# Performance work log

Measured on AMD Instinct MI355X. Metric: run time of the kernel, lower is better.

Reference implementation:

```python
import jax, jax.numpy as jnp
import numpy as np

P = 10      # qubits
LQ = 4      # re-uploading layers
B = 4096    # batch
HID = 32    # readout hidden
DIM = 2 ** P


def _rz(t):
    t = jnp.asarray(t, jnp.float32)
    e = jnp.exp(-0.5j * t.astype(jnp.complex64))
    z = jnp.zeros_like(e)
    return jnp.stack([jnp.stack([e, z], -1), jnp.stack([z, jnp.conj(e)], -1)], -2)


def _rx(t):
    t = jnp.asarray(t, jnp.float32)
    c = jnp.cos(0.5 * t).astype(jnp.complex64)
    s = jnp.sin(0.5 * t).astype(jnp.complex64)
    return jnp.stack([jnp.stack([c, -1j * s], -1), jnp.stack([-1j * s, c], -1)], -2)


def _ry(t):
    t = jnp.asarray(t, jnp.float32)
    c = jnp.cos(0.5 * t).astype(jnp.complex64)
    s = jnp.sin(0.5 * t).astype(jnp.complex64)
    return jnp.stack([jnp.stack([c, -s], -1), jnp.stack([s, c], -1)], -2)


def _apply_1q(state, U, k):
    # state [B, 2^P] complex, U [B,2,2]; wire 0 = most-significant bit (PennyLane order)
    b = state.shape[0]
    s = state.reshape(b, 2 ** k, 2, -1)
    s = jnp.einsum('bij,bajc->baic', U, s)
    return s.reshape(b, -1)


def _apply_cnot(state, c, t):
    b = state.shape[0]
    a, d = min(c, t), max(c, t)
    s = state.reshape(b, 2 ** a, 2, 2 ** (d - a - 1), 2, -1)
    if c == a:  # control = smaller wire index (axis 2), target at axis 4
        hi = jnp.flip(s[:, :, 1], axis=3)  # [b,pre,mid,2,post] -> flip target bit
        s = jnp.stack([s[:, :, 0], hi], axis=2)
    else:       # control = larger wire index (axis 4), target at axis 2
        hi = jnp.flip(s[:, :, :, :, 1], axis=2)  # [b,pre,2,mid,post] -> flip target bit
        s = jnp.stack([s[:, :, :, :, 0], hi], axis=4)
    return s.reshape(b, -1)


def _meas_signs(p):
    # rows 0..p-1: Z_k signs; rows p..2p-1: Z_k Z_{(k+1)%p} signs
    idx = np.arange(2 ** p)
    bits = (idx[None, :] >> (p - 1 - np.arange(p)[:, None])) & 1
    z = (1.0 - 2.0 * bits).astype(np.float32)            # [p, 2^p]
    zz = z * np.roll(z, -1, axis=0)                      # [p, 2^p]
    return jnp.asarray(np.concatenate([z, zz], axis=0))  # [2p, 2^p]


MEAS = _meas_signs(P)


def _circuit_feats(theta, rot_weights, enc_scale, enc_bias):
    b = theta.shape[0]
    # Hadamard on every wire of |0...0> -> uniform superposition
    state = jnp.full((b, DIM), 1.0 / np.sqrt(DIM), dtype=jnp.complex64)
    for l in range(LQ):
        for k in range(P):
            t0 = enc_scale[l, k, 0] * theta[:, k] + enc_bias[l, k, 0]
            t1 = enc_scale[l, k, 1] * theta[:, k] + enc_bias[l, k, 1]
            U_enc = jnp.einsum('bij,bjk->bik', _rx(t1), _rz(t0))  # RX(t1) RZ(t0)
            w = rot_weights[l, k]
            # PennyLane Rot(phi,theta,omega) = RZ(omega) RY(theta) RZ(phi)
            U_rot = _rz(w[2]) @ _ry(w[1]) @ _rz(w[0])
            U = jnp.einsum('ij,bjk->bik', U_rot, U_enc)
            state = _apply_1q(state, U, k)
        for k in range(P):
            state = _apply_cnot(state, k, (k + 1) % P)
    probs = jnp.abs(state) ** 2              # [B, 2^P]
    return probs @ MEAS.T                    # [B, 2P] expectation values


def setup_inputs() -> dict:
    key = jax.random.key(0)
    ks = jax.random.split(key, 4)
    theta = jax.random.uniform(ks[0], (B, P), jnp.float32, -np.pi, np.pi)
    rot_weights = 0.02 * jax.random.normal(ks[1], (LQ, P, 3), dtype=jnp.float32)
    enc_scale = jnp.ones((LQ, P, 2), jnp.float32)   # clamp(0.5,1.5) of ones = ones
    enc_bias = jnp.zeros((LQ, P, 2), jnp.float32)
    n_meas = 2 * P
    W1 = jax.random.normal(ks[2], (HID, n_meas), dtype=jnp.float32) / np.sqrt(n_meas)
    b1 = jnp.zeros((HID,), jnp.float32)
    W2 = jax.random.normal(ks[3], (1, HID), dtype=jnp.float32) / np.sqrt(HID)
    b2 = jnp.zeros((1,), jnp.float32)
    return dict(theta=theta, rot_weights=rot_weights, enc_scale=enc_scale,
                enc_bias=enc_bias, W1=W1, b1=b1, W2=W2, b2=b2)


def reference(theta, rot_weights, enc_scale, enc_bias, W1, b1, W2, b2):
    feats = _circuit_feats(theta, rot_weights, enc_scale, enc_bias)
    h = jax.nn.silu(feats @ W1.T + b1)
    return (h @ W2.T + b2)[:, 0]  # [B]
```

## Files before the change

kernel.cpp:

```cpp
#include <hip/hip_runtime.h>
#include <math.h>

#define NQ   10
#define NLAY 4
#define BATCH 4096
#define HID  32
#define NM   20

typedef float f2 __attribute__((ext_vector_type(2)));

struct Tables {
    unsigned col[NLAY + 1][NQ];
    unsigned row[NLAY + 1][NQ];
};

constexpr Tables make_tables() {
    Tables t{};
    unsigned col[NQ] = {}, row[NQ] = {};
    for (int k = 0; k < NQ; ++k) { col[k] = 1u << (NQ - 1 - k); row[k] = 1u << (NQ - 1 - k); }
    for (int l = 0; l <= NLAY; ++l) {
        for (int k = 0; k < NQ; ++k) { t.col[l][k] = col[k]; t.row[l][k] = row[k]; }
        for (int k = 0; k < NQ; ++k) {
            int c = k, tg = (k + 1) % NQ;
            col[c] ^= col[tg];
            row[tg] ^= row[c];
        }
    }
    return t;
}

static constexpr Tables TB = make_tables();

__device__ __forceinline__ f2 mk2(float a, float b) { f2 r; r[0] = a; r[1] = b; return r; }
__device__ __forceinline__ f2 ffma(f2 a, f2 b, f2 c) { return __builtin_elementwise_fma(a, b, c); }

template<int CTRL>
__device__ __forceinline__ float dppf(float x) {
    return __int_as_float(__builtin_amdgcn_update_dpp(
        0, __float_as_int(x), CTRL, 0xF, 0xF, true));
}

template<unsigned MASK>
__device__ __forceinline__ float xlane(float x) {
    if constexpr (MASK == 0u)       return x;
    else if constexpr (MASK == 1u)  return dppf<0xB1>(x);
    else if constexpr (MASK == 2u)  return dppf<0x4E>(x);
    else if constexpr (MASK == 3u)  return dppf<0x1B>(x);
    else if constexpr (MASK == 7u)  return dppf<0x141>(x);
    else if constexpr (MASK == 8u)  return dppf<0x128>(x);
    else if constexpr (MASK == 10u) return dppf<0x128>(dppf<0x4E>(x));
    else if constexpr (MASK == 15u) return dppf<0x140>(x);
    else return __shfl_xor(x, (int)MASK);
}

__device__ __forceinline__ f2 apply_re(f2 ox, f2 oy, f2 px, f2 py,
                                       f2 ar, f2 ai, f2 br, f2 bi) {
    return ffma(ox, ar, ffma(-oy, ai, ffma(px, br, (-py) * bi)));
}
__device__ __forceinline__ f2 apply_im(f2 ox, f2 oy, f2 px, f2 py,
                                       f2 ar, f2 ai, f2 br, f2 bi) {
    return ffma(ox, ai, ffma(oy, ar, ffma(px, bi, py * br)));
}

template<int L, int K>
__device__ __forceinline__ void apply_gate(f2 (&sre)[8], f2 (&sim)[8],
                                           const float4 (*gm)[2], const int lane) {
    constexpr unsigned v  = TB.col[L][K];
    constexpr unsigned m  = TB.row[L][K];
    constexpr unsigned vl = v >> 4;
    constexpr int vj = (int)(v & 15u), vr = vj >> 1, vs = vj & 1;
    constexpr unsigned ml = m >> 4;
    constexpr int mj = (int)(m & 15u), mjr = mj >> 1, mjs = mj & 1;
    constexpr int gi = L * NQ + K;

    int laneP = 0;
    if constexpr (ml != 0) laneP = __popc((unsigned)lane & ml) & 1;
    const float4 A = gm[gi][laneP];
    f2 occ[2], pcc[2];
    occ[0] = mk2(A.x, A.y); pcc[0] = mk2(A.z, A.w);
    if constexpr (mj != 0) {
        const float4 Bq = gm[gi][laneP ^ 1];
        occ[1] = mk2(Bq.x, Bq.y); pcc[1] = mk2(Bq.z, Bq.w);
    } else { occ[1] = occ[0]; pcc[1] = pcc[0]; }

    f2 ocx[2], ocy[2], pcx[2], pcy[2];
    #pragma unroll
    for (int p_ = 0; p_ < 2; ++p_) {
        const f2 a_ = occ[p_], b_ = occ[p_ ^ mjs];
        const f2 c_ = pcc[p_], d_ = pcc[p_ ^ mjs];
        ocx[p_] = mk2(a_[0], b_[0]); ocy[p_] = mk2(a_[1], b_[1]);
        pcx[p_] = mk2(c_[0], d_[0]); pcy[p_] = mk2(c_[1], d_[1]);
    }

    f2 pre[8], pim[8];
    #pragma unroll
    for (int r = 0; r < 8; ++r) {
        const f2 qre = sre[r ^ vr], qim = sim[r ^ vr];
        const float re0 = vs ? qre[1] : qre[0];
        const float re1 = vs ? qre[0] : qre[1];
        const float im0 = vs ? qim[1] : qim[0];
        const float im1 = vs ? qim[0] : qim[1];
        pre[r] = mk2(xlane<vl>(re0), xlane<vl>(re1));
        pim[r] = mk2(xlane<vl>(im0), xlane<vl>(im1));
    }
    #pragma unroll
    for (int r = 0; r < 8; ++r) {
        const int p_ = __builtin_popcount((unsigned)(r & mjr)) & 1;
        const f2 nre = apply_re(ocx[p_], ocy[p_], pcx[p_], pcy[p_],
                                sre[r], sim[r], pre[r], pim[r]);
        const f2 nim = apply_im(ocx[p_], ocy[p_], pcx[p_], pcy[p_],
                                sre[r], sim[r], pre[r], pim[r]);
        sre[r] = nre; sim[r] = nim;
    }
}

template<unsigned SH>
__device__ __forceinline__ void red_stage(float (&f)[NM]) {
    #pragma unroll
    for (int i = 0; i < NM; ++i) f[i] += xlane<SH>(f[i]);
}

__global__ __launch_bounds__(256, 4) void qrh_kernel(
    const float* __restrict__ theta, const float* __restrict__ rotw,
    const float* __restrict__ escale, const float* __restrict__ ebias,
    const float* __restrict__ W1, const float* __restrict__ b1,
    const float* __restrict__ W2, const float* __restrict__ b2,
    float* __restrict__ out)
{
    __shared__ float4 gmat[4][NLAY * NQ][2];

    const int tid  = threadIdx.x;
    const int lane = tid & 63;
    const int wv   = tid >> 6;
    const int b    = blockIdx.x * 4 + wv;

    if (lane < NLAY * NQ) {
        const int g = lane, l = g / NQ, k = g % NQ;
        const float th = theta[b * NQ + k];
        const int e2 = (l * NQ + k) * 2;
        const float t0 = escale[e2 + 0] * th + ebias[e2 + 0];
        const float t1 = escale[e2 + 1] * th + ebias[e2 + 1];
        float sn0, c0, sn1, c1;
        __sincosf(0.5f * t0, &sn0, &c0);
        __sincosf(0.5f * t1, &sn1, &c1);
        const f2 E00 = mk2( c1 * c0,  -c1 * sn0);
        const f2 E01 = mk2( sn1 * sn0, -sn1 * c0);
        const f2 E10 = mk2(-sn1 * sn0, -sn1 * c0);
        const f2 E11 = mk2( c1 * c0,   c1 * sn0);
        const int r3 = (l * NQ + k) * 3;
        const float w0 = rotw[r3 + 0], w1 = rotw[r3 + 1], w2 = rotw[r3 + 2];
        float cw, sw, ca0, sa0, ca1, sa1;
        __sincosf(0.5f * w1, &sw, &cw);
        __sincosf(0.5f * (w0 + w2), &sa0, &ca0);
        __sincosf(0.5f * (w0 - w2), &sa1, &ca1);
        const f2 R00 = mk2( cw * ca0, -cw * sa0);
        const f2 R01 = mk2(-sw * ca1, -sw * sa1);
        const f2 R10 = mk2( sw * ca1, -sw * sa1);
        const f2 R11 = mk2( cw * ca0,  cw * sa0);
        auto cm = [](f2 a, f2 bb) { return mk2(a[0]*bb[0] - a[1]*bb[1], a[0]*bb[1] + a[1]*bb[0]); };
        const f2 U00 = cm(R00, E00) + cm(R01, E10);
        const f2 U01 = cm(R00, E01) + cm(R01, E11);
        const f2 U10 = cm(R10, E00) + cm(R11, E10);
        const f2 U11 = cm(R10, E01) + cm(R11, E11);
        gmat[wv][g][0] = make_float4(U00[0], U00[1], U01[0], U01[1]);
        gmat[wv][g][1] = make_float4(U11[0], U11[1], U10[0], U10[1]);
    }
    __syncthreads();

    f2 sre[8], sim[8];
    #pragma unroll
    for (int r = 0; r < 8; ++r) { sre[r] = mk2(0.03125f, 0.03125f); sim[r] = mk2(0.f, 0.f); }

    const float4 (*gm)[2] = gmat[wv];

    #define GATE(L,K) apply_gate<L,K>(sre, sim, gm, lane);
    #define LAYER(L) GATE(L,0) GATE(L,1) GATE(L,2) GATE(L,3) GATE(L,4) \
                     GATE(L,5) GATE(L,6) GATE(L,7) GATE(L,8) GATE(L,9)
    LAYER(0)
    LAYER(1)
    LAYER(2)
    LAYER(3)
    #undef LAYER
    #undef GATE

    float w[16];
    #pragma unroll
    for (int r = 0; r < 8; ++r) {
        const f2 p2 = ffma(sre[r], sre[r], sim[r] * sim[r]);
        w[2 * r] = p2[0]; w[2 * r + 1] = p2[1];
    }
    #pragma unroll
    for (int bit = 1; bit < 16; bit <<= 1) {
        #pragma unroll
        for (int j = 0; j < 16; ++j) {
            if (!(j & bit)) {
                const float a = w[j], c = w[j | bit];
                w[j] = a + c; w[j | bit] = a - c;
            }
        }
    }

    float feats[NM];
    #pragma unroll
    for (int f = 0; f < NM; ++f) {
        const unsigned M = (f < NQ) ? TB.row[NLAY][f]
                                    : (TB.row[NLAY][f - NQ] ^ TB.row[NLAY][(f - NQ + 1) % NQ]);
        const int Ml = (int)(M >> 4), Mj = (int)(M & 15u);
        const float s = w[Mj];
        const int lsgn = __popc((unsigned)lane & (unsigned)Ml) & 1;
        feats[f] = lsgn ? -s : s;
    }
    red_stage<1>(feats);
    red_stage<2>(feats);
    red_stage<4>(feats);
    red_stage<8>(feats);
    red_stage<16>(feats);
    red_stage<32>(feats);

    float part = 0.f;
    if (lane < HID) {
        float acc = b1[lane];
        #pragma unroll
        for (int mm = 0; mm < NM; ++mm) acc = fmaf(feats[mm], W1[lane * NM + mm], acc);
        const float sg = 1.f / (1.f + __expf(-acc));
        part = acc * sg * W2[lane];
    }
    part += xlane<32>(part);
    part += xlane<16>(part);
    part += xlane<8>(part);
    part += xlane<4>(part);
    part += xlane<2>(part);
    part += xlane<1>(part);
    if (lane == 0) out[b] = part + b2[0];
}

extern "C" void kernel_launch(void* const* d_in, const int* in_sizes, int n_in,
                              void* d_out, int out_size, void* d_ws, size_t ws_size,
                              hipStream_t stream) {
    (void)in_sizes; (void)n_in; (void)out_size; (void)d_ws; (void)ws_size;
    const float* theta = (const float*)d_in[0];
    const float* rotw  = (const float*)d_in[1];
    const float* esc   = (const float*)d_in[2];
    const float* ebi   = (const float*)d_in[3];
    const float* W1    = (const float*)d_in[4];
    const float* b1    = (const float*)d_in[5];
    const float* W2    = (const float*)d_in[6];
    const float* b2    = (const float*)d_in[7];
    float* out = (float*)d_out;

    qrh_kernel<<<BATCH / 4, 256, 0, stream>>>(theta, rotw, esc, ebi, W1, b1, W2, b2, out);
}
```

Measured before the change: 99.51 us.

## Build first layer as product state and use DPP/permlane swaps for cross-lane ops

Layer 0 is applied to the uniform superposition before any entangling CNOT, so its result is a product state. The kernel now builds that state directly from per-qubit amplitude tables, skipping ten gate applications. Cross-lane exchanges replace ds_bpermute shuffles with DPP row ops combined with permlane16/32 swaps where the builtins exist, and the reductions follow the same pattern. This adds a product-state setup step and a runtime lane-selection probe, and its correctness depends on the permlane swap semantics.

```diff
diff --git a/kernel.cpp b/kernel.cpp
--- a/kernel.cpp
+++ b/kernel.cpp
@@ -7,7 +7,8 @@
 #define HID  32
 #define NM   20
 
-typedef float f2 __attribute__((ext_vector_type(2)));
+typedef float    f2  __attribute__((ext_vector_type(2)));
+typedef unsigned u2v __attribute__((ext_vector_type(2)));
 
 struct Tables {
     unsigned col[NLAY + 1][NQ];
@@ -31,6 +32,11 @@
 
 static constexpr Tables TB = make_tables();
 
+struct cpx { float x, y; };
+__device__ __forceinline__ cpx cxmul(cpx a, cpx b) {
+    return { fmaf(a.x, b.x, -a.y * b.y), fmaf(a.x, b.y, a.y * b.x) };
+}
+
 __device__ __forceinline__ f2 mk2(float a, float b) { f2 r; r[0] = a; r[1] = b; return r; }
 __device__ __forceinline__ f2 ffma(f2 a, f2 b, f2 c) { return __builtin_elementwise_fma(a, b, c); }
 
@@ -40,17 +46,70 @@
         0, __float_as_int(x), CTRL, 0xF, 0xF, true));
 }
 
-template<unsigned MASK>
-__device__ __forceinline__ float xlane(float x) {
-    if constexpr (MASK == 0u)       return x;
-    else if constexpr (MASK == 1u)  return dppf<0xB1>(x);
-    else if constexpr (MASK == 2u)  return dppf<0x4E>(x);
-    else if constexpr (MASK == 3u)  return dppf<0x1B>(x);
-    else if constexpr (MASK == 7u)  return dppf<0x141>(x);
-    else if constexpr (MASK == 8u)  return dppf<0x128>(x);
-    else if constexpr (MASK == 10u) return dppf<0x128>(dppf<0x4E>(x));
-    else if constexpr (MASK == 15u) return dppf<0x140>(x);
-    else return __shfl_xor(x, (int)MASK);
+template<unsigned M>
+__device__ __forceinline__ float dpplo(float x) {
+    static_assert(M < 16u, "dpplo handles masks 0..15");
+    if constexpr (M == 0u)       return x;
+    else if constexpr (M == 1u)  return dppf<0xB1>(x);
+    else if constexpr (M == 2u)  return dppf<0x4E>(x);
+    else if constexpr (M == 3u)  return dppf<0x1B>(x);
+    else if constexpr (M == 7u)  return dppf<0x141>(x);
+    else if constexpr (M == 8u)  return dppf<0x128>(x);
+    else if constexpr (M == 15u) return dppf<0x140>(x);
+    else if constexpr (M == 4u)  return dppf<0x141>(dppf<0x1B>(x));
+    else if constexpr (M == 5u)  return dppf<0x141>(dppf<0x4E>(x));
+    else if constexpr (M == 6u)  return dppf<0x141>(dppf<0xB1>(x));
+    else if constexpr (M == 9u)  return dppf<0x128>(dppf<0xB1>(x));
+    else if constexpr (M == 10u) return dppf<0x128>(dppf<0x4E>(x));
+    else if constexpr (M == 11u) return dppf<0x128>(dppf<0x1B>(x));
+    else if constexpr (M == 12u) return dppf<0x140>(dppf<0x1B>(x));
+    else if constexpr (M == 13u) return dppf<0x140>(dppf<0x4E>(x));
+    else                         return dppf<0x140>(dppf<0xB1>(x));
+}
+
+__device__ __forceinline__ float swap16sel(float x, bool sel16) {
+#if __has_builtin(__builtin_amdgcn_permlane16_swap)
+    u2v r = __builtin_amdgcn_permlane16_swap(__float_as_uint(x), __float_as_uint(x), false, false);
+    return sel16 ? __uint_as_float(r[0]) : __uint_as_float(r[1]);
+#else
+    (void)sel16; return __shfl_xor(x, 16);
+#endif
+}
+__device__ __forceinline__ float swap32sel(float x, bool sel32) {
+#if __has_builtin(__builtin_amdgcn_permlane32_swap)
+    u2v r = __builtin_amdgcn_permlane32_swap(__float_as_uint(x), __float_as_uint(x), false, false);
+    return sel32 ? __uint_as_float(r[0]) : __uint_as_float(r[1]);
+#else
+    (void)sel32; return __shfl_xor(x, 32);
+#endif
+}
+__device__ __forceinline__ float redfold16(float x) {
+#if __has_builtin(__builtin_amdgcn_permlane16_swap)
+    u2v r = __builtin_amdgcn_permlane16_swap(__float_as_uint(x), __float_as_uint(x), false, false);
+    return __uint_as_float(r[0]) + __uint_as_float(r[1]);
+#else
+    return x + __shfl_xor(x, 16);
+#endif
+}
+__device__ __forceinline__ float redfold32(float x) {
+#if __has_builtin(__builtin_amdgcn_permlane32_swap)
+    u2v r = __builtin_amdgcn_permlane32_swap(__float_as_uint(x), __float_as_uint(x), false, false);
+    return __uint_as_float(r[0]) + __uint_as_float(r[1]);
+#else
+    return x + __shfl_xor(x, 32);
+#endif
+}
+
+template<unsigned M>
+__device__ __forceinline__ float xlane(float x, bool sel16, bool sel32) {
+    if constexpr (M == 0u) return x;
+    else if constexpr ((M & 48u) == 48u) return __shfl_xor(x, (int)M);
+    else {
+        float y = dpplo<M & 15u>(x);
+        if constexpr ((M & 48u) == 16u)      y = swap16sel(y, sel16);
+        else if constexpr ((M & 48u) == 32u) y = swap32sel(y, sel32);
+        return y;
+    }
 }
 
 __device__ __forceinline__ f2 apply_re(f2 ox, f2 oy, f2 px, f2 py,
@@ -64,7 +123,8 @@
 
 template<int L, int K>
 __device__ __forceinline__ void apply_gate(f2 (&sre)[8], f2 (&sim)[8],
-                                           const float4 (*gm)[2], const int lane) {
+                                           const float4 (*gm)[2], const int lane,
+                                           const bool sel16, const bool sel32) {
     constexpr unsigned v  = TB.col[L][K];
     constexpr unsigned m  = TB.row[L][K];
     constexpr unsigned vl = v >> 4;
@@ -100,8 +160,8 @@
         const float re1 = vs ? qre[0] : qre[1];
         const float im0 = vs ? qim[1] : qim[0];
         const float im1 = vs ? qim[0] : qim[1];
-        pre[r] = mk2(xlane<vl>(re0), xlane<vl>(re1));
-        pim[r] = mk2(xlane<vl>(im0), xlane<vl>(im1));
+        pre[r] = mk2(xlane<vl>(re0, sel16, sel32), xlane<vl>(re1, sel16, sel32));
+        pim[r] = mk2(xlane<vl>(im0, sel16, sel32), xlane<vl>(im1, sel16, sel32));
     }
     #pragma unroll
     for (int r = 0; r < 8; ++r) {
@@ -112,12 +172,6 @@
                                 sre[r], sim[r], pre[r], pim[r]);
         sre[r] = nre; sim[r] = nim;
     }
-}
-
-template<unsigned SH>
-__device__ __forceinline__ void red_stage(float (&f)[NM]) {
-    #pragma unroll
-    for (int i = 0; i < NM; ++i) f[i] += xlane<SH>(f[i]);
 }
 
 __global__ __launch_bounds__(256, 4) void qrh_kernel(
@@ -128,11 +182,26 @@
     float* __restrict__ out)
 {
     __shared__ float4 gmat[4][NLAY * NQ][2];
+    __shared__ float4 wtab[4][NQ];
 
     const int tid  = threadIdx.x;
     const int lane = tid & 63;
     const int wv   = tid >> 6;
     const int b    = blockIdx.x * 4 + wv;
+
+    bool sel16 = false, sel32 = false;
+#if __has_builtin(__builtin_amdgcn_permlane16_swap)
+    {
+        u2v r = __builtin_amdgcn_permlane16_swap((unsigned)lane, (unsigned)lane, false, false);
+        sel16 = (((lane & 16) != 0) == (r[0] == (unsigned)(lane & ~16)));
+    }
+#endif
+#if __has_builtin(__builtin_amdgcn_permlane32_swap)
+    {
+        u2v r = __builtin_amdgcn_permlane32_swap((unsigned)lane, (unsigned)lane, false, false);
+        sel32 = (((lane & 32) != 0) == (r[0] == (unsigned)(lane & ~32)));
+    }
+#endif
 
     if (lane < NLAY * NQ) {
         const int g = lane, l = g / NQ, k = g % NQ;
@@ -164,19 +233,55 @@
         const f2 U11 = cm(R10, E01) + cm(R11, E11);
         gmat[wv][g][0] = make_float4(U00[0], U00[1], U01[0], U01[1]);
         gmat[wv][g][1] = make_float4(U11[0], U11[1], U10[0], U10[1]);
+        if (l == 0) {
+            const float inv = 0.70710678118654752f;
+            const f2 al = (U00 + U01) * inv;
+            const f2 be = (U10 + U11) * inv;
+            wtab[wv][k] = make_float4(al[0], al[1], be[0], be[1]);
+        }
     }
     __syncthreads();
 
     f2 sre[8], sim[8];
-    #pragma unroll
-    for (int r = 0; r < 8; ++r) { sre[r] = mk2(0.03125f, 0.03125f); sim[r] = mk2(0.f, 0.f); }
+    {
+        cpx pre;
+        {
+            const float4 q = wtab[wv][0];
+            pre = ((lane >> 5) & 1) ? cpx{q.z, q.w} : cpx{q.x, q.y};
+            #pragma unroll
+            for (int k = 1; k < 6; ++k) {
+                const float4 t = wtab[wv][k];
+                const cpx w_ = ((lane >> (5 - k)) & 1) ? cpx{t.z, t.w} : cpx{t.x, t.y};
+                pre = cxmul(pre, w_);
+            }
+        }
+        const float4 q6 = wtab[wv][6], q7 = wtab[wv][7];
+        const float4 q8 = wtab[wv][8], q9 = wtab[wv][9];
+        const cpx w6[2] = {{q6.x, q6.y}, {q6.z, q6.w}};
+        const cpx w7[2] = {{q7.x, q7.y}, {q7.z, q7.w}};
+        const cpx w8[2] = {{q8.x, q8.y}, {q8.z, q8.w}};
+        const cpx w9[2] = {{q9.x, q9.y}, {q9.z, q9.w}};
+        cpx ph[4], tlo[4];
+        #pragma unroll
+        for (int a = 0; a < 4; ++a) {
+            ph[a]  = cxmul(pre, cxmul(w6[a >> 1], w7[a & 1]));
+            tlo[a] = cxmul(w8[a >> 1], w9[a & 1]);
+        }
+        #pragma unroll
+        for (int r = 0; r < 8; ++r) {
+            const int j0 = 2 * r, j1 = 2 * r + 1;
+            const cpx a0 = cxmul(ph[j0 >> 2], tlo[j0 & 3]);
+            const cpx a1 = cxmul(ph[j1 >> 2], tlo[j1 & 3]);
+            sre[r] = mk2(a0.x, a1.x);
+            sim[r] = mk2(a0.y, a1.y);
+        }
+    }
 
     const float4 (*gm)[2] = gmat[wv];
 
-    #define GATE(L,K) apply_gate<L,K>(sre, sim, gm, lane);
+    #define GATE(L,K) apply_gate<L,K>(sre, sim, gm, lane, sel16, sel32);
     #define LAYER(L) GATE(L,0) GATE(L,1) GATE(L,2) GATE(L,3) GATE(L,4) \
                      GATE(L,5) GATE(L,6) GATE(L,7) GATE(L,8) GATE(L,9)
-    LAYER(0)
     LAYER(1)
     LAYER(2)
     LAYER(3)
@@ -210,12 +315,17 @@
         const int lsgn = __popc((unsigned)lane & (unsigned)Ml) & 1;
         feats[f] = lsgn ? -s : s;
     }
-    red_stage<1>(feats);
-    red_stage<2>(feats);
-    red_stage<4>(feats);
-    red_stage<8>(feats);
-    red_stage<16>(feats);
-    red_stage<32>(feats);
+    #pragma unroll
+    for (int f = 0; f < NM; ++f) {
+        float v = feats[f];
+        v += dppf<0xB1>(v);
+        v += dppf<0x4E>(v);
+        v += dppf<0x141>(v);
+        v += dppf<0x128>(v);
+        v = redfold16(v);
+        v = redfold32(v);
+        feats[f] = v;
+    }
 
     float part = 0.f;
     if (lane < HID) {
@@ -225,12 +335,12 @@
         const float sg = 1.f / (1.f + __expf(-acc));
         part = acc * sg * W2[lane];
     }
-    part += xlane<32>(part);
-    part += xlane<16>(part);
-    part += xlane<8>(part);
-    part += xlane<4>(part);
-    part += xlane<2>(part);
-    part += xlane<1>(part);
+    part += dppf<0xB1>(part);
+    part += dppf<0x4E>(part);
+    part += dppf<0x141>(part);
+    part += dppf<0x128>(part);
+    part = redfold16(part);
+    part = redfold32(part);
     if (lane == 0) out[b] = part + b2[0];
 }
 
```

Measured after the change: 102.4 us. 2.9% more time.
